# Kernel optimization log

Measured on AMD Instinct MI355X. Metric: run time of the kernel, lower is better.

Reference implementation:

```python
import jax, jax.numpy as jnp
import numpy as np
import math

B, S, H, L, N, V = 4, 2048, 1024, 4, 4, 256
D = H // N
EPS = 1e-5


def setup_inputs() -> dict:
    key = jax.random.key(0)
    ks = iter(jax.random.split(key, 40))
    sc = 1.0 / math.sqrt(H)
    def w(shape, s=None):
        return jax.random.normal(next(ks), shape, dtype=jnp.float32) * (s if s is not None else sc)
    inp = {
        "input_ids": jax.random.randint(next(ks), (B, S), 0, V, dtype=jnp.int32),
        "embed": w((V, H), 0.02),
        "nm_gate_w": w((H, H)), "nm_gate_b": jnp.zeros((H,), jnp.float32),
        "nm_filter_w": w((H, H)), "nm_filter_b": jnp.zeros((H,), jnp.float32),
        "nm_ctx_w": w((2, H)), "nm_ctx_b": jnp.zeros((2,), jnp.float32),
        "q_w": w((L, H, H)), "q_b": jnp.zeros((L, H), jnp.float32),
        "k_w": w((L, H, H)), "k_b": jnp.zeros((L, H), jnp.float32),
        "v_w": w((L, H, H)), "v_b": jnp.zeros((L, H), jnp.float32),
        "gain_w": w((L, N, H)), "gain_b": jnp.zeros((L, N), jnp.float32),
        "attn_ow": w((L, H, H)), "attn_ob": jnp.zeros((L, H), jnp.float32),
        "en_w": w((L, H, H)), "en_b": jnp.zeros((L, H), jnp.float32),
        "plastic_w": w((L, H, H)),
        "fix_w": w((L, H, H)), "fix_b": jnp.zeros((L, H), jnp.float32),
        "ln_g": jnp.ones((L, H), jnp.float32), "ln_b": jnp.zeros((L, H), jnp.float32),
        "out_w": w((V, H)), "out_b": jnp.zeros((V,), jnp.float32),
    }
    return inp


def _forward(input_ids, embed, nm_gate_w, nm_gate_b, nm_filter_w, nm_filter_b,
             nm_ctx_w, nm_ctx_b, q_w, q_b, k_w, k_b, v_w, v_b, gain_w, gain_b,
             attn_ow, attn_ob, en_w, en_b, plastic_w, fix_w, fix_b, ln_g, ln_b,
             out_w, out_b):
    x = embed[input_ids]                                   # [B,S,H]
    # --- NeurotransmitterModule ---
    ctx = x.mean(axis=1)                                   # [B,H]
    nm = ctx @ nm_ctx_w.T + nm_ctx_b                       # [B,2]
    dop, nor = nm[:, :1], nm[:, 1:]                        # [B,1] each
    gate = jax.nn.sigmoid(x @ nm_gate_w.T + nm_gate_b)
    x = x * (1.0 + dop[:, None, :] * gate)
    noise = jnp.tanh(x @ nm_filter_w.T + nm_filter_b)
    x = x + nor[:, None, :] * noise
    inv_sqrt_d = 1.0 / math.sqrt(D)
    for l in range(L):
        # --- GainControlAttention ---
        q = (x @ q_w[l].T + q_b[l]).reshape(B, S, N, D).transpose(0, 2, 1, 3)
        k = (x @ k_w[l].T + k_b[l]).reshape(B, S, N, D).transpose(0, 2, 1, 3)
        v = (x @ v_w[l].T + v_b[l]).reshape(B, S, N, D).transpose(0, 2, 1, 3)
        gain = x.mean(axis=1) @ gain_w[l].T + gain_b[l]    # [B,N]
        q = q * (1.0 + gain[:, :, None, None])
        scores = jnp.einsum('bnsd,bntd->bnst', q, k) * inv_sqrt_d
        attn = jax.nn.softmax(scores, axis=-1)
        ctxv = jnp.einsum('bnst,bntd->bnsd', attn, v)
        a = ctxv.transpose(0, 2, 1, 3).reshape(B, S, H) @ attn_ow[l].T + attn_ob[l]
        x = x + a
        # --- EnergyConstrainedLayer ---
        x = jax.nn.silu(x @ en_w[l].T + en_b[l])
        # --- NeuroplasticityLayer (eval mode) ---
        x = x + (x @ fix_w[l].T + fix_b[l]) + (x @ plastic_w[l].T)
        # --- LayerNorm ---
        mu = x.mean(axis=-1, keepdims=True)
        var = jnp.mean((x - mu) ** 2, axis=-1, keepdims=True)
        x = (x - mu) * jax.lax.rsqrt(var + EPS) * ln_g[l] + ln_b[l]
    return x @ out_w.T + out_b                             # [B,S,V]


def reference(input_ids, embed, nm_gate_w, nm_gate_b, nm_filter_w, nm_filter_b,
              nm_ctx_w, nm_ctx_b, q_w, q_b, k_w, k_b, v_w, v_b, gain_w, gain_b,
              attn_ow, attn_ob, en_w, en_b, plastic_w, fix_w, fix_b, ln_g, ln_b,
              out_w, out_b):
    return _forward(input_ids, embed, nm_gate_w, nm_gate_b, nm_filter_w,
                    nm_filter_b, nm_ctx_w, nm_ctx_b, q_w, q_b, k_w, k_b, v_w,
                    v_b, gain_w, gain_b, attn_ow, attn_ob, en_w, en_b,
                    plastic_w, fix_w, fix_b, ln_g, ln_b, out_w, out_b)
```

## Files before the change

kernel.cpp:

```cpp
#include <hip/hip_runtime.h>

#define B_ 4
#define S_ 2048
#define H_ 1024
#define L_ 4
#define N_ 4
#define D_ 256
#define V_ 256
#define EPSF 1e-5f
#define WH_ ((size_t)H_ * H_)

typedef __attribute__((ext_vector_type(8))) short short8;
typedef __attribute__((ext_vector_type(4))) float f32x4;

__device__ inline float bf2f(unsigned short u) {
    union { unsigned int ui; float f; } c; c.ui = ((unsigned int)u) << 16; return c.f;
}
__device__ inline unsigned short f2bf(float f) {
    union { float f; unsigned int ui; } c; c.f = f;
    unsigned int u = c.ui;
    unsigned int r = (u + 0x7FFFu + ((u >> 16) & 1u)) >> 16;
    return (unsigned short)r;
}
__device__ inline float wave64_sum(float v) {
    for (int m = 32; m >= 1; m >>= 1) v += __shfl_xor(v, m, 64);
    return v;
}
__device__ inline void gl_lds16(const unsigned short* g, unsigned short* l) {
    __builtin_amdgcn_global_load_lds(
        (const __attribute__((address_space(1))) unsigned int*)g,
        (__attribute__((address_space(3))) unsigned int*)l, 16, 0, 0);
}

__global__ void wcvt_kernel(const float* __restrict__ W,
                            unsigned short* __restrict__ Wb, int n8) {
    int idx = blockIdx.x * 256 + threadIdx.x;
    if (idx >= n8) return;
    size_t base = (size_t)idx * 8;
    float4 a0 = *(const float4*)(W + base);
    float4 a1 = *(const float4*)(W + base + 4);
    short8 t;
    t[0] = f2bf(a0.x); t[1] = f2bf(a0.y); t[2] = f2bf(a0.z); t[3] = f2bf(a0.w);
    t[4] = f2bf(a1.x); t[5] = f2bf(a1.y); t[6] = f2bf(a1.z); t[7] = f2bf(a1.w);
    *(short8*)(Wb + base) = t;
}

__global__ void wcvt_qkv(const float* __restrict__ W,
                         unsigned short* __restrict__ Wb, int n8, int sel) {
    int idx = blockIdx.x * 256 + threadIdx.x;
    if (idx >= n8) return;
    size_t p = (size_t)idx * 8;
    size_t layer = p >> 20;
    size_t within = p & (WH_ - 1);
    size_t dst = layer * 3 * WH_ + (size_t)sel * WH_ + within;
    float4 a0 = *(const float4*)(W + p);
    float4 a1 = *(const float4*)(W + p + 4);
    short8 t;
    t[0] = f2bf(a0.x); t[1] = f2bf(a0.y); t[2] = f2bf(a0.z); t[3] = f2bf(a0.w);
    t[4] = f2bf(a1.x); t[5] = f2bf(a1.y); t[6] = f2bf(a1.z); t[7] = f2bf(a1.w);
    *(short8*)(Wb + dst) = t;
}

__global__ void wadd_kernel(const float* __restrict__ Wa, const float* __restrict__ Wb2,
                            unsigned short* __restrict__ Wo, int n8) {
    int idx = blockIdx.x * 256 + threadIdx.x;
    if (idx >= n8) return;
    size_t base = (size_t)idx * 8;
    short8 t;
#pragma unroll
    for (int e = 0; e < 8; e++) {
        size_t p = base + e;
        int pos = (int)(p & (WH_ - 1));
        float v = Wa[p] + Wb2[p] + (((pos >> 10) == (pos & (H_ - 1))) ? 1.f : 0.f);
        t[e] = f2bf(v);
    }
    *(short8*)(Wo + base) = t;
}

__global__ void gather_kernel(const int* __restrict__ ids,
                              const float* __restrict__ embed,
                              unsigned short* __restrict__ x) {
    size_t idx = (size_t)blockIdx.x * 256 + threadIdx.x;
    int bs = (int)(idx >> 10);
    int h  = (int)(idx & 1023);
    x[idx] = f2bf(embed[(size_t)ids[bs] * H_ + h]);
}

__global__ void mean_kernel(const unsigned short* __restrict__ Xin,
                            float* __restrict__ xmean) {
    int idx = blockIdx.x * 256 + threadIdx.x;
    int b = idx >> 10, h = idx & 1023;
    int s0 = blockIdx.y * 128;
    const unsigned short* p = Xin + ((size_t)b * S_ + s0) * H_ + h;
    float s = 0.f;
    for (int i = 0; i < 128; i++) s += bf2f(p[(size_t)i * H_]);
    atomicAdd(&xmean[idx], s);
}

__global__ void nm_kernel(const float* __restrict__ xmean,
                          const float* __restrict__ w,
                          const float* __restrict__ bias,
                          float* __restrict__ dopnor) {
    int wave = threadIdx.x >> 6, lane = threadIdx.x & 63;
    for (int p = wave; p < 2 * B_; p += 4) {
        int b = p >> 1, j = p & 1;
        float s = 0.f;
        for (int h = lane; h < H_; h += 64) s += xmean[b * H_ + h] * w[j * H_ + h];
        s = wave64_sum(s);
        if (lane == 0) dopnor[p] = s / (float)S_ + bias[j];
    }
}

__global__ void gain_kernel(const float* __restrict__ xmean,
                            const float* __restrict__ gw,
                            const float* __restrict__ gb,
                            float* __restrict__ qscale) {
    int wave = threadIdx.x >> 6, lane = threadIdx.x & 63;
    for (int p = wave; p < B_ * N_; p += 4) {
        int b = p >> 2, n = p & 3;
        float s = 0.f;
        for (int h = lane; h < H_; h += 64) s += xmean[b * H_ + h] * gw[n * H_ + h];
        s = wave64_sum(s);
        if (lane == 0) qscale[p] = (1.f + s / (float)S_ + gb[n]) * 0.0625f;
    }
}

__global__ __launch_bounds__(256) void gemm_bt(
    const unsigned short* __restrict__ A, const unsigned short* __restrict__ W,
    const float* __restrict__ bias, void* __restrict__ Cout,
    const unsigned short* __restrict__ X, const float* __restrict__ scal,
    int K, int Nout, int mode) {
    __shared__ unsigned short As[128 * 32];
    __shared__ unsigned short Bs[128 * 32];
    int tid = threadIdx.x;
    int wave = tid >> 6, lane = tid & 63;
    int quad = lane >> 4, l16 = lane & 15;
    int bm = blockIdx.x * 128;
    int bn = blockIdx.y * 128;
    int mw = (wave >> 1) * 64, nw = (wave & 1) * 64;

    const unsigned short* Ag = A + (size_t)(bm + wave * 16 + (lane >> 2)) * K + (lane & 3) * 8;
    const unsigned short* Wg = W + (size_t)(bn + wave * 16 + (lane >> 2)) * K + (lane & 3) * 8;
    unsigned short* ldsA = As + wave * 512;
    unsigned short* ldsB = Bs + wave * 512;
    size_t rowskip = (size_t)64 * K;

    f32x4 acc[4][4];
#pragma unroll
    for (int i = 0; i < 4; i++)
#pragma unroll
        for (int j = 0; j < 4; j++)
#pragma unroll
            for (int r = 0; r < 4; r++) acc[i][j][r] = 0.f;

    for (int kk = 0; kk < K; kk += 32) {
        __syncthreads();
        gl_lds16(Ag + kk, ldsA);
        gl_lds16(Ag + rowskip + kk, ldsA + 2048);
        gl_lds16(Wg + kk, ldsB);
        gl_lds16(Wg + rowskip + kk, ldsB + 2048);
        __syncthreads();

        short8 af[4], bfr[4];
#pragma unroll
        for (int i = 0; i < 4; i++)
            af[i] = *(const short8*)&As[(mw + i * 16 + l16) * 32 + quad * 8];
#pragma unroll
        for (int j = 0; j < 4; j++)
            bfr[j] = *(const short8*)&Bs[(nw + j * 16 + l16) * 32 + quad * 8];
#pragma unroll
        for (int i = 0; i < 4; i++)
#pragma unroll
            for (int j = 0; j < 4; j++)
                acc[i][j] = __builtin_amdgcn_mfma_f32_16x16x32_bf16(af[i], bfr[j], acc[i][j], 0, 0, 0);
    }

    if (mode == 6) {
#pragma unroll
        for (int i = 0; i < 4; i++) {
#pragma unroll
            for (int j = 0; j < 4; j++) {
                int col = bn + nw + j * 16 + l16;
                float bv = bias ? bias[col] : 0.f;
                int n = col >> 8, d = col & 255;
                int row0 = bm + mw + i * 16 + quad * 4;
                int b = row0 >> 11, s0 = row0 & 2047;
                union { unsigned short u[4]; uint2 v; } pk;
#pragma unroll
                for (int r = 0; r < 4; r++) pk.u[r] = f2bf(acc[i][j][r] + bv);
                *(uint2*)((unsigned short*)Cout +
                          ((size_t)(b * N_ + n) * D_ + d) * S_ + s0) = pk.v;
            }
        }
        return;
    }

#pragma unroll
    for (int i = 0; i < 4; i++) {
#pragma unroll
        for (int j = 0; j < 4; j++) {
            int col = bn + nw + j * 16 + l16;
            float bv = bias ? bias[col] : 0.f;
#pragma unroll
            for (int r = 0; r < 4; r++) {
                int row = bm + mw + i * 16 + quad * 4 + r;
                float v = acc[i][j][r] + bv;
                size_t off = (size_t)row * Nout + col;
                if (mode == 5) {
                    ((float*)Cout)[off] = v;
                    continue;
                }
                float outv;
                if (mode == 0) {
                    outv = v;
                } else if (mode == 1) {
                    float sig = 1.f / (1.f + __expf(-v));
                    float dop = scal[(row >> 11) * 2];
                    outv = bf2f(X[off]) * (1.f + dop * sig);
                } else if (mode == 2) {
                    float nor = scal[(row >> 11) * 2 + 1];
                    outv = bf2f(X[off]) + nor * tanhf(v);
                } else if (mode == 3) {
                    outv = v + bf2f(X[off]);
                } else {
                    outv = v * (1.f / (1.f + __expf(-v)));
                }
                ((unsigned short*)Cout)[off] = f2bf(outv);
            }
        }
    }
}

__global__ __launch_bounds__(256) void gemm_qkv(
    const unsigned short* __restrict__ A, const unsigned short* __restrict__ W,
    const float* __restrict__ qb, const float* __restrict__ kb,
    const float* __restrict__ vbb, unsigned short* __restrict__ Qo,
    unsigned short* __restrict__ Ko, unsigned short* __restrict__ Vt) {
    __shared__ unsigned short As[128 * 32];
    __shared__ unsigned short Bs[128 * 32];
    const int K = H_;
    int tid = threadIdx.x;
    int wave = tid >> 6, lane = tid & 63;
    int quad = lane >> 4, l16 = lane & 15;
    int bm = blockIdx.x * 128;
    int bn = blockIdx.y * 128;
    int mw = (wave >> 1) * 64, nw = (wave & 1) * 64;

    const unsigned short* Ag = A + (size_t)(bm + wave * 16 + (lane >> 2)) * K + (lane & 3) * 8;
    const unsigned short* Wg = W + (size_t)(bn + wave * 16 + (lane >> 2)) * K + (lane & 3) * 8;
    unsigned short* ldsA = As + wave * 512;
    unsigned short* ldsB = Bs + wave * 512;
    size_t rowskip = (size_t)64 * K;

    f32x4 acc[4][4];
#pragma unroll
    for (int i = 0; i < 4; i++)
#pragma unroll
        for (int j = 0; j < 4; j++)
#pragma unroll
            for (int r = 0; r < 4; r++) acc[i][j][r] = 0.f;

    for (int kk = 0; kk < K; kk += 32) {
        __syncthreads();
        gl_lds16(Ag + kk, ldsA);
        gl_lds16(Ag + rowskip + kk, ldsA + 2048);
        gl_lds16(Wg + kk, ldsB);
        gl_lds16(Wg + rowskip + kk, ldsB + 2048);
        __syncthreads();

        short8 af[4], bfr[4];
#pragma unroll
        for (int i = 0; i < 4; i++)
            af[i] = *(const short8*)&As[(mw + i * 16 + l16) * 32 + quad * 8];
#pragma unroll
        for (int j = 0; j < 4; j++)
            bfr[j] = *(const short8*)&Bs[(nw + j * 16 + l16) * 32 + quad * 8];
#pragma unroll
        for (int i = 0; i < 4; i++)
#pragma unroll
            for (int j = 0; j < 4; j++)
                acc[i][j] = __builtin_amdgcn_mfma_f32_16x16x32_bf16(af[i], bfr[j], acc[i][j], 0, 0, 0);
    }

    int sel = (bn + nw) >> 10;
    if (sel == 2) {
#pragma unroll
        for (int i = 0; i < 4; i++) {
#pragma unroll
            for (int j = 0; j < 4; j++) {
                int c2 = ((bn + nw) & 1023) + j * 16 + l16;
                float bv = vbb[c2];
                int n = c2 >> 8, d = c2 & 255;
                int row0 = bm + mw + i * 16 + quad * 4;
                int b = row0 >> 11, s0 = row0 & 2047;
                union { unsigned short u[4]; uint2 v; } pk;
#pragma unroll
                for (int r = 0; r < 4; r++) pk.u[r] = f2bf(acc[i][j][r] + bv);
                *(uint2*)(Vt + ((size_t)(b * N_ + n) * D_ + d) * S_ + s0) = pk.v;
            }
        }
    } else {
        unsigned short* Co = (sel == 0) ? Qo : Ko;
        const float* bias = (sel == 0) ? qb : kb;
#pragma unroll
        for (int i = 0; i < 4; i++) {
#pragma unroll
            for (int j = 0; j < 4; j++) {
                int c2 = ((bn + nw) & 1023) + j * 16 + l16;
                float bv = bias[c2];
#pragma unroll
                for (int r = 0; r < 4; r++) {
                    int row = bm + mw + i * 16 + quad * 4 + r;
                    Co[(size_t)row * H_ + c2] = f2bf(acc[i][j][r] + bv);
                }
            }
        }
    }
}

__global__ __launch_bounds__(512) void flash_attn(
    const unsigned short* __restrict__ Q, const unsigned short* __restrict__ Kg,
    const unsigned short* __restrict__ VT, const float* __restrict__ qscale,
    unsigned short* __restrict__ O) {
    __shared__ unsigned short Kt[64][264];
    __shared__ unsigned short Vtl[272][72];
    __shared__ unsigned short Pl[8][16][72];

    int tid = threadIdx.x;
    int wave = tid >> 6, lane = tid & 63;
    int quad = lane >> 4, l16 = lane & 15;
    int bnh = blockIdx.y;
    size_t base = ((size_t)(bnh >> 2) * S_) * H_ + (size_t)(bnh & 3) * D_;
    size_t vtbase = (size_t)bnh * D_ * S_;
    int qw = blockIdx.x * 128 + wave * 16;
    float scale = qscale[bnh];

    for (int c = tid; c < 16 * 72; c += 512) {
        int rr = c / 72, cc = c - rr * 72;
        Vtl[256 + rr][cc] = (rr == 0) ? (unsigned short)0x3F80 : (unsigned short)0;
    }

    short8 qf[8];
#pragma unroll
    for (int kk = 0; kk < 8; kk++)
        qf[kk] = *(const short8*)(Q + base +
            (size_t)(qw + l16) * H_ + kk * 32 + quad * 8);

    f32x4 o[16], osum;
#pragma unroll
    for (int c = 0; c < 16; c++)
#pragma unroll
        for (int r = 0; r < 4; r++) o[c][r] = 0.f;
#pragma unroll
    for (int r = 0; r < 4; r++) osum[r] = 0.f;
    float mrow[4];
#pragma unroll
    for (int r = 0; r < 4; r++) mrow[r] = -1e30f;

    for (int t0 = 0; t0 < S_; t0 += 64) {
        __syncthreads();
#pragma unroll
        for (int rr = 0; rr < 4; rr++) {
            int c = rr * 512 + tid;
            int row = c >> 5, col = (c & 31) * 8;
            *(short8*)&Kt[row][col] =
                *(const short8*)(Kg + base + (size_t)(t0 + row) * H_ + col);
        }
#pragma unroll
        for (int rr = 0; rr < 4; rr++) {
            int c = rr * 512 + tid;
            int d = c >> 3, col = (c & 7) * 8;
            *(short8*)&Vtl[d][col] =
                *(const short8*)(VT + vtbase + (size_t)d * S_ + t0 + col);
        }
        __syncthreads();

        f32x4 s[4];
#pragma unroll
        for (int j = 0; j < 4; j++)
#pragma unroll
            for (int r = 0; r < 4; r++) s[j][r] = 0.f;
#pragma unroll
        for (int j = 0; j < 4; j++)
#pragma unroll
            for (int kk = 0; kk < 8; kk++) {
                short8 kf = *(const short8*)&Kt[j * 16 + l16][kk * 32 + quad * 8];
                s[j] = __builtin_amdgcn_mfma_f32_16x16x32_bf16(qf[kk], kf, s[j], 0, 0, 0);
            }

        float sv[4][4], mx[4];
        bool ok = true;
#pragma unroll
        for (int r = 0; r < 4; r++) {
#pragma unroll
            for (int j = 0; j < 4; j++) sv[r][j] = s[j][r] * scale;
            float m0 = fmaxf(fmaxf(sv[r][0], sv[r][1]), fmaxf(sv[r][2], sv[r][3]));
            for (int m = 8; m >= 1; m >>= 1) m0 = fmaxf(m0, __shfl_xor(m0, m, 64));
            mx[r] = m0;
            ok = ok && (m0 <= mrow[r] + 8.f);
        }
        if (__all(ok)) {
#pragma unroll
            for (int r = 0; r < 4; r++)
#pragma unroll
                for (int j = 0; j < 4; j++)
                    Pl[wave][quad * 4 + r][j * 16 + l16] =
                        f2bf(__expf(sv[r][j] - mrow[r]));
        } else {
            float alpha[4];
#pragma unroll
            for (int r = 0; r < 4; r++) {
                float mnew = fmaxf(mrow[r], mx[r]);
                alpha[r] = __expf(mrow[r] - mnew);
                mrow[r] = mnew;
#pragma unroll
                for (int j = 0; j < 4; j++)
                    Pl[wave][quad * 4 + r][j * 16 + l16] =
                        f2bf(__expf(sv[r][j] - mnew));
            }
#pragma unroll
            for (int c = 0; c < 16; c++)
#pragma unroll
                for (int r = 0; r < 4; r++) o[c][r] *= alpha[r];
#pragma unroll
            for (int r = 0; r < 4; r++) osum[r] *= alpha[r];
        }

        short8 pf0 = *(const short8*)&Pl[wave][l16][quad * 8];
        short8 pf1 = *(const short8*)&Pl[wave][l16][32 + quad * 8];
#pragma unroll
        for (int c = 0; c < 16; c++) {
            short8 vf0 = *(const short8*)&Vtl[c * 16 + l16][quad * 8];
            o[c] = __builtin_amdgcn_mfma_f32_16x16x32_bf16(pf0, vf0, o[c], 0, 0, 0);
            short8 vf1 = *(const short8*)&Vtl[c * 16 + l16][32 + quad * 8];
            o[c] = __builtin_amdgcn_mfma_f32_16x16x32_bf16(pf1, vf1, o[c], 0, 0, 0);
        }
        {
            short8 vs0 = *(const short8*)&Vtl[256 + l16][quad * 8];
            short8 vs1 = *(const short8*)&Vtl[256 + l16][32 + quad * 8];
            osum = __builtin_amdgcn_mfma_f32_16x16x32_bf16(pf0, vs0, osum, 0, 0, 0);
            osum = __builtin_amdgcn_mfma_f32_16x16x32_bf16(pf1, vs1, osum, 0, 0, 0);
        }
    }

    float invl[4];
#pragma unroll
    for (int r = 0; r < 4; r++)
        invl[r] = 1.f / __shfl(osum[r], (lane & 48), 64);
#pragma unroll
    for (int c = 0; c < 16; c++)
#pragma unroll
        for (int r = 0; r < 4; r++) {
            int row = qw + quad * 4 + r;
            int d = c * 16 + l16;
            O[base + (size_t)row * H_ + d] = f2bf(o[c][r] * invl[r]);
        }
}

__global__ __launch_bounds__(256) void ln_kernel(
    const unsigned short* __restrict__ y, const float* __restrict__ g,
    const float* __restrict__ bta, unsigned short* __restrict__ out) {
    int row = blockIdx.x;
    size_t ro = (size_t)row * H_;
    int tid = threadIdx.x;
    float t[4]; float s = 0.f, s2 = 0.f;
#pragma unroll
    for (int i = 0; i < 4; i++) {
        int h = i * 256 + tid;
        float v = bf2f(y[ro + h]);
        t[i] = v; s += v; s2 += v * v;
    }
    s = wave64_sum(s); s2 = wave64_sum(s2);
    __shared__ float sh[8];
    int wave = tid >> 6, lane = tid & 63;
    if (lane == 0) { sh[wave] = s; sh[4 + wave] = s2; }
    __syncthreads();
    s  = sh[0] + sh[1] + sh[2] + sh[3];
    s2 = sh[4] + sh[5] + sh[6] + sh[7];
    float mu = s * (1.f / H_);
    float var = s2 * (1.f / H_) - mu * mu;
    float inv = rsqrtf(var + EPSF);
#pragma unroll
    for (int i = 0; i < 4; i++) {
        int h = i * 256 + tid;
        out[ro + h] = f2bf((t[i] - mu) * inv * g[h] + bta[h]);
    }
}

extern "C" void kernel_launch(void* const* d_in, const int* in_sizes, int n_in,
                              void* d_out, int out_size, void* d_ws, size_t ws_size,
                              hipStream_t stream) {
    const int*   ids          = (const int*)d_in[0];
    const float* embed        = (const float*)d_in[1];
    const float* nm_gate_w    = (const float*)d_in[2];
    const float* nm_gate_b    = (const float*)d_in[3];
    const float* nm_filter_w  = (const float*)d_in[4];
    const float* nm_filter_b  = (const float*)d_in[5];
    const float* nm_ctx_w     = (const float*)d_in[6];
    const float* nm_ctx_b     = (const float*)d_in[7];
    const float* q_w          = (const float*)d_in[8];
    const float* q_b          = (const float*)d_in[9];
    const float* k_w          = (const float*)d_in[10];
    const float* k_b          = (const float*)d_in[11];
    const float* v_w          = (const float*)d_in[12];
    const float* v_b          = (const float*)d_in[13];
    const float* gain_w       = (const float*)d_in[14];
    const float* gain_b       = (const float*)d_in[15];
    const float* attn_ow      = (const float*)d_in[16];
    const float* attn_ob      = (const float*)d_in[17];
    const float* en_w         = (const float*)d_in[18];
    const float* en_b         = (const float*)d_in[19];
    const float* plastic_w    = (const float*)d_in[20];
    const float* fix_w        = (const float*)d_in[21];
    const float* fix_b        = (const float*)d_in[22];
    const float* ln_g         = (const float*)d_in[23];
    const float* ln_b         = (const float*)d_in[24];
    const float* out_w        = (const float*)d_in[25];
    const float* out_b        = (const float*)d_in[26];

    size_t T  = (size_t)B_ * S_ * H_;
    size_t smallBytes = ((size_t)B_ * H_ + 2 * B_ + B_ * N_ + 8) * sizeof(float);
    size_t megaElems  = 26 * WH_ + WH_ / 4;
    size_t need_base  = 4 * T * 2 + smallBytes + 2 * WH_;
    size_t need_mega  = 4 * T * 2 + smallBytes + 2 * megaElems;
    if (ws_size < need_base) return;
    bool mega = ws_size >= need_mega;

    unsigned short* X   = (unsigned short*)d_ws;
    unsigned short* Qb  = X + T;
    unsigned short* Kb  = Qb + T;
    unsigned short* Vb  = Kb + T;
    float* xmean  = (float*)(Vb + T);
    float* dopnor = xmean + (size_t)B_ * H_;
    float* qscale = dopnor + 2 * B_;
    unsigned short* Wbase = (unsigned short*)(qscale + B_ * N_ + 8);
#define WOFF(k) (Wbase + (size_t)(k) * WH_)

    const int M   = B_ * S_;
    const int W8  = (int)(WH_ / 8);
    const int WG  = (W8 + 255) / 256;
    const int W84 = (int)(4 * WH_ / 8);
    const int WG4 = (W84 + 255) / 256;
    const int W8o = V_ * H_ / 8;
    const int WGo = (W8o + 255) / 256;

    if (mega) {
        wcvt_kernel<<<WG,  256, 0, stream>>>(nm_gate_w,   WOFF(0), W8);
        wcvt_kernel<<<WG,  256, 0, stream>>>(nm_filter_w, WOFF(1), W8);
        wcvt_qkv<<<WG4, 256, 0, stream>>>(q_w, WOFF(2), W84, 0);
        wcvt_qkv<<<WG4, 256, 0, stream>>>(k_w, WOFF(2), W84, 1);
        wcvt_qkv<<<WG4, 256, 0, stream>>>(v_w, WOFF(2), W84, 2);
        wcvt_kernel<<<WG4, 256, 0, stream>>>(attn_ow, WOFF(14), W84);
        wcvt_kernel<<<WG4, 256, 0, stream>>>(en_w,    WOFF(18), W84);
        wadd_kernel<<<WG4, 256, 0, stream>>>(fix_w, plastic_w, WOFF(22), W84);
        wcvt_kernel<<<WGo, 256, 0, stream>>>(out_w, WOFF(26), W8o);
    }

    gather_kernel<<<dim3((int)(T / 256)), 256, 0, stream>>>(ids, embed, X);

    hipMemsetAsync(xmean, 0, (size_t)B_ * H_ * sizeof(float), stream);
    mean_kernel<<<dim3(B_ * H_ / 256, 16), 256, 0, stream>>>(X, xmean);
    nm_kernel<<<1, 256, 0, stream>>>(xmean, nm_ctx_w, nm_ctx_b, dopnor);

    const unsigned short* Wp;
    if (mega) Wp = WOFF(0);
    else { wcvt_kernel<<<WG, 256, 0, stream>>>(nm_gate_w, Wbase, W8); Wp = Wbase; }
    gemm_bt<<<dim3(M / 128, H_ / 128), 256, 0, stream>>>(
        X, Wp, nm_gate_b, Qb, X, dopnor, H_, H_, 1);
    if (mega) Wp = WOFF(1);
    else { wcvt_kernel<<<WG, 256, 0, stream>>>(nm_filter_w, Wbase, W8); Wp = Wbase; }
    gemm_bt<<<dim3(M / 128, H_ / 128), 256, 0, stream>>>(
        Qb, Wp, nm_filter_b, X, Qb, dopnor, H_, H_, 2);

    for (int l = 0; l < L_; l++) {
        size_t wo = (size_t)l * WH_;
        size_t bo = (size_t)l * H_;
        hipMemsetAsync(xmean, 0, (size_t)B_ * H_ * sizeof(float), stream);
        mean_kernel<<<dim3(B_ * H_ / 256, 16), 256, 0, stream>>>(X, xmean);
        gain_kernel<<<1, 256, 0, stream>>>(xmean, gain_w + (size_t)l * N_ * H_,
                                           gain_b + (size_t)l * N_, qscale);

        if (mega) {
            gemm_qkv<<<dim3(M / 128, 3 * H_ / 128), 256, 0, stream>>>(
                X, WOFF(2) + (size_t)l * 3 * WH_, q_b + bo, k_b + bo, v_b + bo,
                Qb, Kb, Vb);
        } else {
            wcvt_kernel<<<WG, 256, 0, stream>>>(q_w + wo, Wbase, W8);
            gemm_bt<<<dim3(M / 128, H_ / 128), 256, 0, stream>>>(
                X, Wbase, q_b + bo, Qb, nullptr, nullptr, H_, H_, 0);
            wcvt_kernel<<<WG, 256, 0, stream>>>(k_w + wo, Wbase, W8);
            gemm_bt<<<dim3(M / 128, H_ / 128), 256, 0, stream>>>(
                X, Wbase, k_b + bo, Kb, nullptr, nullptr, H_, H_, 0);
            wcvt_kernel<<<WG, 256, 0, stream>>>(v_w + wo, Wbase, W8);
            gemm_bt<<<dim3(M / 128, H_ / 128), 256, 0, stream>>>(
                X, Wbase, v_b + bo, Vb, nullptr, nullptr, H_, H_, 6);
        }

        flash_attn<<<dim3(S_ / 128, B_ * N_), 512, 0, stream>>>(
            Qb, Kb, Vb, qscale, Qb);

        if (mega) Wp = WOFF(14) + wo;
        else { wcvt_kernel<<<WG, 256, 0, stream>>>(attn_ow + wo, Wbase, W8); Wp = Wbase; }
        gemm_bt<<<dim3(M / 128, H_ / 128), 256, 0, stream>>>(
            Qb, Wp, attn_ob + bo, Kb, X, nullptr, H_, H_, 3);
        if (mega) Wp = WOFF(18) + wo;
        else { wcvt_kernel<<<WG, 256, 0, stream>>>(en_w + wo, Wbase, W8); Wp = Wbase; }
        gemm_bt<<<dim3(M / 128, H_ / 128), 256, 0, stream>>>(
            Kb, Wp, en_b + bo, Vb, nullptr, nullptr, H_, H_, 4);
        if (mega) Wp = WOFF(22) + wo;
        else { wadd_kernel<<<WG, 256, 0, stream>>>(fix_w + wo, plastic_w + wo, Wbase, W8); Wp = Wbase; }
        gemm_bt<<<dim3(M / 128, H_ / 128), 256, 0, stream>>>(
            Vb, Wp, fix_b + bo, Qb, nullptr, nullptr, H_, H_, 0);
        ln_kernel<<<dim3(M), 256, 0, stream>>>(Qb, ln_g + bo, ln_b + bo, X);
    }

    if (mega) Wp = WOFF(26);
    else { wcvt_kernel<<<WGo, 256, 0, stream>>>(out_w, Wbase, W8o); Wp = Wbase; }
    gemm_bt<<<dim3(M / 128, V_ / 128), 256, 0, stream>>>(
        X, Wp, out_b, (float*)d_out, nullptr, nullptr, H_, V_, 5);
#undef WOFF
}
```

Measured before the change: 1.789 ms.

## Double-buffer K/V tiles in flash attention via async global-to-LDS loads with XOR swizzle

The flash attention kernel now prefetches the next K and V tiles into a second LDS buffer with direct global-to-LDS loads (gl_lds16) while the current tile is computed, and needs only one barrier per iteration. Padded LDS layouts are replaced by unpadded buffers using an XOR swizzle to avoid bank conflicts, and the ones-row used for row sums moves to its own small array. This is meant to hide global load latency behind the MFMA work. In exchange LDS use roughly doubles, which may lower occupancy.

Result: no change. 1.773 ms (-0.9%).

```diff
diff --git a/kernel.cpp b/kernel.cpp
--- a/kernel.cpp
+++ b/kernel.cpp
@@ -322,13 +322,15 @@
     const unsigned short* __restrict__ Q, const unsigned short* __restrict__ Kg,
     const unsigned short* __restrict__ VT, const float* __restrict__ qscale,
     unsigned short* __restrict__ O) {
-    __shared__ unsigned short Kt[64][264];
-    __shared__ unsigned short Vtl[272][72];
+    __shared__ unsigned short Kb[2][64 * 256];
+    __shared__ unsigned short Vb[2][256 * 64];
+    __shared__ unsigned short Vones[16][72];
     __shared__ unsigned short Pl[8][16][72];
 
     int tid = threadIdx.x;
     int wave = tid >> 6, lane = tid & 63;
     int quad = lane >> 4, l16 = lane & 15;
+    int rx = l16 & 7;
     int bnh = blockIdx.y;
     size_t base = ((size_t)(bnh >> 2) * S_) * H_ + (size_t)(bnh & 3) * D_;
     size_t vtbase = (size_t)bnh * D_ * S_;
@@ -337,8 +339,14 @@
 
     for (int c = tid; c < 16 * 72; c += 512) {
         int rr = c / 72, cc = c - rr * 72;
-        Vtl[256 + rr][cc] = (rr == 0) ? (unsigned short)0x3F80 : (unsigned short)0;
-    }
+        Vones[rr][cc] = (rr == 0) ? (unsigned short)0x3F80 : (unsigned short)0;
+    }
+
+    int l5 = lane >> 5;
+    int ks = lane & 31;
+    int vrow = lane >> 3;
+    int vs = lane & 7;
+    int vmask = vrow & 7;
 
     short8 qf[8];
 #pragma unroll
@@ -357,23 +365,49 @@
 #pragma unroll
     for (int r = 0; r < 4; r++) mrow[r] = -1e30f;
 
+    {
+#pragma unroll
+        for (int k = 0; k < 4; k++) {
+            int chunk = 4 * wave + k;
+            int kmask = (2 * k + l5) & 7;
+            int grow = 2 * chunk + l5;
+            int gcol = ((ks ^ kmask)) * 8;
+            gl_lds16(Kg + base + (size_t)grow * H_ + gcol, &Kb[0][chunk * 512]);
+        }
+#pragma unroll
+        for (int k = 0; k < 4; k++) {
+            int chunk = 4 * wave + k;
+            int d = 8 * chunk + vrow;
+            int gcol = ((vs ^ vmask)) * 8;
+            gl_lds16(VT + vtbase + (size_t)d * S_ + gcol, &Vb[0][chunk * 512]);
+        }
+    }
+    asm volatile("s_waitcnt vmcnt(0)" ::: "memory");
+    __syncthreads();
+
+    int cur = 0;
     for (int t0 = 0; t0 < S_; t0 += 64) {
-        __syncthreads();
-#pragma unroll
-        for (int rr = 0; rr < 4; rr++) {
-            int c = rr * 512 + tid;
-            int row = c >> 5, col = (c & 31) * 8;
-            *(short8*)&Kt[row][col] =
-                *(const short8*)(Kg + base + (size_t)(t0 + row) * H_ + col);
-        }
-#pragma unroll
-        for (int rr = 0; rr < 4; rr++) {
-            int c = rr * 512 + tid;
-            int d = c >> 3, col = (c & 7) * 8;
-            *(short8*)&Vtl[d][col] =
-                *(const short8*)(VT + vtbase + (size_t)d * S_ + t0 + col);
-        }
-        __syncthreads();
+        if (t0 + 64 < S_) {
+            int nb = cur ^ 1;
+#pragma unroll
+            for (int k = 0; k < 4; k++) {
+                int chunk = 4 * wave + k;
+                int kmask = (2 * k + l5) & 7;
+                int grow = t0 + 64 + 2 * chunk + l5;
+                int gcol = ((ks ^ kmask)) * 8;
+                gl_lds16(Kg + base + (size_t)grow * H_ + gcol, &Kb[nb][chunk * 512]);
+            }
+#pragma unroll
+            for (int k = 0; k < 4; k++) {
+                int chunk = 4 * wave + k;
+                int d = 8 * chunk + vrow;
+                int gcol = ((vs ^ vmask)) * 8;
+                gl_lds16(VT + vtbase + (size_t)d * S_ + t0 + 64 + gcol, &Vb[nb][chunk * 512]);
+            }
+        }
+
+        const unsigned short* Kc = Kb[cur];
+        const unsigned short* Vc = Vb[cur];
 
         f32x4 s[4];
 #pragma unroll
@@ -384,7 +418,8 @@
         for (int j = 0; j < 4; j++)
 #pragma unroll
             for (int kk = 0; kk < 8; kk++) {
-                short8 kf = *(const short8*)&Kt[j * 16 + l16][kk * 32 + quad * 8];
+                short8 kf = *(const short8*)&Kc[(j * 16 + l16) * 256 +
+                                                ((4 * kk + quad) ^ rx) * 8];
                 s[j] = __builtin_amdgcn_mfma_f32_16x16x32_bf16(qf[kk], kf, s[j], 0, 0, 0);
             }
 
@@ -430,17 +465,21 @@
         short8 pf1 = *(const short8*)&Pl[wave][l16][32 + quad * 8];
 #pragma unroll
         for (int c = 0; c < 16; c++) {
-            short8 vf0 = *(const short8*)&Vtl[c * 16 + l16][quad * 8];
+            short8 vf0 = *(const short8*)&Vc[(c * 16 + l16) * 64 + (quad ^ rx) * 8];
             o[c] = __builtin_amdgcn_mfma_f32_16x16x32_bf16(pf0, vf0, o[c], 0, 0, 0);
-            short8 vf1 = *(const short8*)&Vtl[c * 16 + l16][32 + quad * 8];
+            short8 vf1 = *(const short8*)&Vc[(c * 16 + l16) * 64 + ((4 | quad) ^ rx) * 8];
             o[c] = __builtin_amdgcn_mfma_f32_16x16x32_bf16(pf1, vf1, o[c], 0, 0, 0);
         }
         {
-            short8 vs0 = *(const short8*)&Vtl[256 + l16][quad * 8];
-            short8 vs1 = *(const short8*)&Vtl[256 + l16][32 + quad * 8];
+            short8 vs0 = *(const short8*)&Vones[l16][quad * 8];
+            short8 vs1 = *(const short8*)&Vones[l16][32 + quad * 8];
             osum = __builtin_amdgcn_mfma_f32_16x16x32_bf16(pf0, vs0, osum, 0, 0, 0);
             osum = __builtin_amdgcn_mfma_f32_16x16x32_bf16(pf1, vs1, osum, 0, 0, 0);
         }
+
+        asm volatile("s_waitcnt vmcnt(0)" ::: "memory");
+        __syncthreads();
+        cur ^= 1;
     }
 
     float invl[4];
```
